# Kernel tuning notes

Measured on AMD Instinct MI355X. Metric: run time of the kernel, lower is better.

Reference implementation:

```python
import jax, jax.numpy as jnp
import numpy as np

C = 1.0          # curvature
ALPHA = 0.2      # LeakyReLU negative slope
MIN_NORM = 1e-15
MASK_VAL = -9e15

def artanh(x):
    x = jnp.clip(x, -1 + 1e-7, 1 - 1e-7)
    return 0.5 * (jnp.log1p(x) - jnp.log1p(-x))

def logmap0(x, c):
    sqrt_c = jnp.sqrt(c)
    norm = jnp.maximum(jnp.linalg.norm(x, axis=-1, keepdims=True), MIN_NORM)
    return x / (sqrt_c * norm) * artanh(sqrt_c * norm)

def expmap0(u, c):
    sqrt_c = jnp.sqrt(c)
    norm = jnp.maximum(jnp.linalg.norm(u, axis=-1, keepdims=True), MIN_NORM)
    return jnp.tanh(sqrt_c * norm) * u / (sqrt_c * norm)

def proj(x, c):
    norm = jnp.maximum(jnp.linalg.norm(x, axis=-1, keepdims=True), MIN_NORM)
    maxnorm = (1.0 - 1e-5) / jnp.sqrt(c)
    return jnp.where(norm > maxnorm, x / norm * maxnorm, x)

def setup_inputs() -> dict:
    key = jax.random.key(0)
    k1, k2, k3, k4, k5 = jax.random.split(key, 5)
    N, D, CLS = 8192, 128, 16
    # points on the Poincare ball (small norm, then projected)
    x = proj(jax.random.normal(k1, (N, D), jnp.float32) * 0.01, C)
    # sparse-ish adjacency, avg degree ~32, with self loops
    adj = jax.random.uniform(k2, (N, N)) < (32.0 / N)
    adj = adj | jnp.eye(N, dtype=bool)
    W = jax.random.normal(k3, (D, CLS), jnp.float32) * (1.0 / np.sqrt(D))
    b = jnp.zeros((CLS,), jnp.float32)
    a_src = jax.random.normal(k4, (CLS,), jnp.float32) * 0.1
    a_dst = jax.random.normal(k5, (CLS,), jnp.float32) * 0.1
    return {"x": x, "adj": adj, "W": W, "b": b, "a_src": a_src, "a_dst": a_dst}

def reference(x, adj, W, b, a_src, a_dst):
    # hyperbolic -> tangent space at origin, then linear map to n_classes
    h = logmap0(x, C) @ W + b                              # [N, CLS]
    # GAT scores: e_ij = LeakyReLU(a_src.h_i + a_dst.h_j)
    e = jax.nn.leaky_relu((h @ a_src)[:, None] + (h @ a_dst)[None, :], ALPHA)  # [N, N]
    e = jnp.where(adj, e, MASK_VAL)
    att = jax.nn.softmax(e, axis=-1)                       # row softmax over neighbors
    out = jax.nn.elu(att @ h)                              # aggregate + activation
    # back onto the manifold
    return proj(expmap0(out, C), C)
```

## Files before the change

### kernel.cpp

```cpp
#include <hip/hip_runtime.h>
#include <math.h>

#define NN   8192
#define DD   128
#define CLS  16
#define ALPHA 0.2f
#define MAXD 1024

__global__ void adj_probe(const unsigned char* __restrict__ adj, int* flag)
{
    const int lane = threadIdx.x & 63;
    const int i = lane + 1;
    const int ok = ((i & 3) != 0) && (adj[(size_t)i * (NN + 1)] != 0);
    unsigned long long b = __ballot(ok);
    if (threadIdx.x == 0) *flag = (__popcll(b) > 24) ? 1 : 0;
}

__global__ __launch_bounds__(256) void hat_feat(
    const float* __restrict__ x, const float* __restrict__ W,
    const float* __restrict__ b, const float* __restrict__ a_src,
    const float* __restrict__ a_dst,
    float* __restrict__ h, float* __restrict__ s, float* __restrict__ dv)
{
    const int lane = threadIdx.x & 63;
    const int row  = (blockIdx.x << 2) + (threadIdx.x >> 6);

    const float* xr = x + (size_t)row * DD;
    float x0 = xr[lane];
    float x1 = xr[lane + 64];

    float nsq = x0 * x0 + x1 * x1;
    #pragma unroll
    for (int o = 32; o > 0; o >>= 1) nsq += __shfl_xor(nsq, o);

    float norm = fmaxf(sqrtf(nsq), 1e-15f);
    float t    = fminf(norm, 1.0f - 1e-7f);
    float art  = 0.5f * (log1pf(t) - log1pf(-t));
    float scl  = art / norm;
    x0 *= scl;
    x1 *= scl;

    float hc[CLS];
    #pragma unroll
    for (int c = 0; c < CLS; ++c)
        hc[c] = x0 * W[lane * CLS + c] + x1 * W[(lane + 64) * CLS + c];

    #pragma unroll
    for (int o = 32; o > 0; o >>= 1) {
        #pragma unroll
        for (int c = 0; c < CLS; ++c) hc[c] += __shfl_xor(hc[c], o);
    }

    float sv = 0.0f, dvv = 0.0f;
    #pragma unroll
    for (int c = 0; c < CLS; ++c) {
        hc[c] += b[c];
        sv  += hc[c] * a_src[c];
        dvv += hc[c] * a_dst[c];
    }

    if (lane == 0) {
        float* hr = h + (size_t)row * CLS;
        #pragma unroll
        for (int c = 0; c < CLS; ++c) hr[c] = hc[c];
        s[row]  = sv;
        dv[row] = dvv;
    }
}

__global__ __launch_bounds__(256) void hat_scan(
    const unsigned char* __restrict__ adj, const int* __restrict__ flag,
    int* __restrict__ nbr, int* __restrict__ cnt)
{
    const int lane = threadIdx.x & 63;
    const int row  = (blockIdx.x << 2) + (threadIdx.x >> 6);
    const bool bytemode = (*flag != 0);

    unsigned long long m0 = 0ull, m1 = 0ull;
    if (bytemode) {
        const uint4* arow = reinterpret_cast<const uint4*>(adj + (size_t)row * NN);
        #pragma unroll
        for (int it = 0; it < 8; ++it) {
            const uint4 a = arow[(it << 6) | lane];
            unsigned n0 = ((a.x & 0x01010101u) * 0x01020408u) >> 24;
            unsigned n1 = ((a.y & 0x01010101u) * 0x01020408u) >> 24;
            unsigned n2 = ((a.z & 0x01010101u) * 0x01020408u) >> 24;
            unsigned n3 = ((a.w & 0x01010101u) * 0x01020408u) >> 24;
            unsigned long long bits = (unsigned long long)(
                (n0 & 0xF) | ((n1 & 0xF) << 4) | ((n2 & 0xF) << 8) | ((n3 & 0xF) << 12));
            if (it < 4) m0 |= bits << (it << 4);
            else        m1 |= bits << ((it - 4) << 4);
        }
    } else {
        const uint4* arow = reinterpret_cast<const uint4*>(
            reinterpret_cast<const unsigned int*>(adj) + (size_t)row * NN);
        #pragma unroll
        for (int it = 0; it < 32; ++it) {
            const uint4 a = arow[(it << 6) | lane];
            unsigned long long bits =
                (unsigned long long)((a.x != 0u) | ((a.y != 0u) << 1) |
                                     ((a.z != 0u) << 2) | ((a.w != 0u) << 3));
            if (it < 16) m0 |= bits << (it << 2);
            else         m1 |= bits << ((it - 16) << 2);
        }
    }

    const int c = __popcll(m0) + __popcll(m1);
    int off = c;
    #pragma unroll
    for (int o = 1; o < 64; o <<= 1) {
        int v = __shfl_up(off, o);
        if (lane >= o) off += v;
    }
    const int total = __shfl(off, 63);
    off -= c;

    int* rbase = nbr + (size_t)row * MAXD;
    while (m0) {
        const int b = __builtin_ctzll(m0);
        m0 &= m0 - 1;
        const int j = bytemode ? (((b >> 4) << 10) | (lane << 4) | (b & 15))
                               : (((b >> 2) << 8)  | (lane << 2) | (b & 3));
        if (off < MAXD) rbase[off] = j;
        ++off;
    }
    while (m1) {
        const int b0 = __builtin_ctzll(m1);
        m1 &= m1 - 1;
        const int b = b0 + 64;
        const int j = bytemode ? (((b >> 4) << 10) | (lane << 4) | (b & 15))
                               : (((b >> 2) << 8)  | (lane << 2) | (b & 3));
        if (off < MAXD) rbase[off] = j;
        ++off;
    }
    if (lane == 0) cnt[row] = (total < MAXD) ? total : MAXD;
}

__global__ __launch_bounds__(256) void hat_agg(
    const float* __restrict__ h, const float* __restrict__ s,
    const float* __restrict__ dv, const int* __restrict__ nbr,
    const int* __restrict__ cnt, float* __restrict__ out)
{
    const int lane = threadIdx.x & 63;
    const int row  = (blockIdx.x << 2) + (threadIdx.x >> 6);
    const int cc   = lane & 15;
    const int g    = lane >> 4;

    const int n = cnt[row];
    const int* rbase = nbr + (size_t)row * MAXD;
    const float si = s[row];

    float mx = -3.0e38f;
    for (int i = lane; i < n; i += 64) {
        float e = si + dv[rbase[i]];
        e = (e > 0.0f) ? e : ALPHA * e;
        mx = fmaxf(mx, e);
    }
    #pragma unroll
    for (int o = 32; o > 0; o >>= 1) mx = fmaxf(mx, __shfl_xor(mx, o));

    float l = 0.0f, acc = 0.0f;
    #pragma unroll 2
    for (int base = 0; base < n; base += 4) {
        const int idx = base + g;
        if (idx < n) {
            const int j = rbase[idx];
            float e = si + dv[j];
            e = (e > 0.0f) ? e : ALPHA * e;
            const float w = __expf(e - mx);
            l += w;
            acc = fmaf(w, h[(size_t)j * CLS + cc], acc);
        }
    }
    l   += __shfl_xor(l, 16);   l   += __shfl_xor(l, 32);
    acc += __shfl_xor(acc, 16); acc += __shfl_xor(acc, 32);

    float* orow = out + (size_t)row * CLS;
    if (l > 0.0f) {
        float u = acc / l;
        u = (u > 0.0f) ? u : expm1f(u);
        float nsq = u * u;
        #pragma unroll
        for (int o = 8; o > 0; o >>= 1) nsq += __shfl_xor(nsq, o);
        float norm = fmaxf(sqrtf(nsq), 1e-15f);
        float th   = tanhf(norm);
        float sc2  = th / norm;
        const float maxnorm = 1.0f - 1e-5f;
        float sc3  = (th > maxnorm) ? (maxnorm / th) : 1.0f;
        if (lane < CLS) orow[lane] = u * sc2 * sc3;
    } else {
        if (lane < CLS) orow[lane] = 0.0f;
    }
}

extern "C" void kernel_launch(void* const* d_in, const int* in_sizes, int n_in,
                              void* d_out, int out_size, void* d_ws, size_t ws_size,
                              hipStream_t stream) {
    const float*         x     = (const float*)d_in[0];
    const unsigned char* adj   = (const unsigned char*)d_in[1];
    const float*         W     = (const float*)d_in[2];
    const float*         b     = (const float*)d_in[3];
    const float*         a_src = (const float*)d_in[4];
    const float*         a_dst = (const float*)d_in[5];
    float*               out   = (float*)d_out;

    float* h    = (float*)d_ws;
    float* s    = h + (size_t)NN * CLS;
    float* dv   = s + NN;
    int*   flag = (int*)(dv + NN);
    int*   cnt  = flag + 1;
    int*   nbr  = cnt + NN;

    adj_probe<<<1, 64, 0, stream>>>(adj, flag);
    hat_feat<<<NN / 4, 256, 0, stream>>>(x, W, b, a_src, a_dst, h, s, dv);
    hat_scan<<<NN / 4, 256, 0, stream>>>(adj, flag, nbr, cnt);
    hat_agg <<<NN / 4, 256, 0, stream>>>(h, s, dv, nbr, cnt, out);
}
```

Before: 72.20 us.

## Split adjacency row scan across four waves and fold probe into feature kernel

The adjacency scan now gives each row a full 256-thread block, with each wave handling a quarter of the row and writing to its own neighbor segment and count. This raises parallelism and memory-level concurrency for the scan, which reads the large adjacency matrix. The aggregation kernel walks the four segments in turn. The separate probe kernel is merged into the first block of the feature kernel to save one launch. Each segment holds at most 256 neighbors, so rows with a dense quarter would be truncated.

After: 69.17 us. 4.2% less time.

```diff
diff --git a/kernel.cpp b/kernel.cpp
--- a/kernel.cpp
+++ b/kernel.cpp
@@ -5,25 +5,24 @@
 #define DD   128
 #define CLS  16
 #define ALPHA 0.2f
-#define MAXD 1024
-
-__global__ void adj_probe(const unsigned char* __restrict__ adj, int* flag)
-{
-    const int lane = threadIdx.x & 63;
-    const int i = lane + 1;
-    const int ok = ((i & 3) != 0) && (adj[(size_t)i * (NN + 1)] != 0);
-    unsigned long long b = __ballot(ok);
-    if (threadIdx.x == 0) *flag = (__popcll(b) > 24) ? 1 : 0;
-}
+#define SEGCAP 256
 
 __global__ __launch_bounds__(256) void hat_feat(
     const float* __restrict__ x, const float* __restrict__ W,
     const float* __restrict__ b, const float* __restrict__ a_src,
-    const float* __restrict__ a_dst,
-    float* __restrict__ h, float* __restrict__ s, float* __restrict__ dv)
+    const float* __restrict__ a_dst, const unsigned char* __restrict__ adj,
+    float* __restrict__ h, float* __restrict__ s, float* __restrict__ dv,
+    int* __restrict__ flag)
 {
     const int lane = threadIdx.x & 63;
     const int row  = (blockIdx.x << 2) + (threadIdx.x >> 6);
+
+    if (blockIdx.x == 0 && threadIdx.x < 64) {
+        const int i = threadIdx.x + 1;
+        const int ok = ((i & 3) != 0) && (adj[(size_t)i * (NN + 1)] != 0);
+        unsigned long long bb = __ballot(ok);
+        if (threadIdx.x == 0) *flag = (__popcll(bb) > 24) ? 1 : 0;
+    }
 
     const float* xr = x + (size_t)row * DD;
     float x0 = xr[lane];
@@ -70,42 +69,41 @@
 
 __global__ __launch_bounds__(256) void hat_scan(
     const unsigned char* __restrict__ adj, const int* __restrict__ flag,
-    int* __restrict__ nbr, int* __restrict__ cnt)
+    int* __restrict__ nbr, int* __restrict__ cnt4)
 {
     const int lane = threadIdx.x & 63;
-    const int row  = (blockIdx.x << 2) + (threadIdx.x >> 6);
+    const int q    = threadIdx.x >> 6;
+    const int row  = blockIdx.x;
     const bool bytemode = (*flag != 0);
 
-    unsigned long long m0 = 0ull, m1 = 0ull;
+    unsigned mask = 0u;
     if (bytemode) {
-        const uint4* arow = reinterpret_cast<const uint4*>(adj + (size_t)row * NN);
-        #pragma unroll
-        for (int it = 0; it < 8; ++it) {
-            const uint4 a = arow[(it << 6) | lane];
+        const uint4* abase = reinterpret_cast<const uint4*>(
+            adj + (size_t)row * NN + q * 2048);
+        #pragma unroll
+        for (int it = 0; it < 2; ++it) {
+            const uint4 a = abase[(it << 6) | lane];
             unsigned n0 = ((a.x & 0x01010101u) * 0x01020408u) >> 24;
             unsigned n1 = ((a.y & 0x01010101u) * 0x01020408u) >> 24;
             unsigned n2 = ((a.z & 0x01010101u) * 0x01020408u) >> 24;
             unsigned n3 = ((a.w & 0x01010101u) * 0x01020408u) >> 24;
-            unsigned long long bits = (unsigned long long)(
-                (n0 & 0xF) | ((n1 & 0xF) << 4) | ((n2 & 0xF) << 8) | ((n3 & 0xF) << 12));
-            if (it < 4) m0 |= bits << (it << 4);
-            else        m1 |= bits << ((it - 4) << 4);
+            unsigned bits = (n0 & 0xF) | ((n1 & 0xF) << 4)
+                          | ((n2 & 0xF) << 8) | ((n3 & 0xF) << 12);
+            mask |= bits << (it << 4);
         }
     } else {
-        const uint4* arow = reinterpret_cast<const uint4*>(
-            reinterpret_cast<const unsigned int*>(adj) + (size_t)row * NN);
-        #pragma unroll
-        for (int it = 0; it < 32; ++it) {
-            const uint4 a = arow[(it << 6) | lane];
-            unsigned long long bits =
-                (unsigned long long)((a.x != 0u) | ((a.y != 0u) << 1) |
-                                     ((a.z != 0u) << 2) | ((a.w != 0u) << 3));
-            if (it < 16) m0 |= bits << (it << 2);
-            else         m1 |= bits << ((it - 16) << 2);
-        }
-    }
-
-    const int c = __popcll(m0) + __popcll(m1);
+        const uint4* abase = reinterpret_cast<const uint4*>(
+            reinterpret_cast<const unsigned int*>(adj) + (size_t)row * NN + q * 2048);
+        #pragma unroll
+        for (int it = 0; it < 8; ++it) {
+            const uint4 a = abase[(it << 6) | lane];
+            unsigned bits = (unsigned)(a.x != 0u)        | ((unsigned)(a.y != 0u) << 1)
+                          | ((unsigned)(a.z != 0u) << 2) | ((unsigned)(a.w != 0u) << 3);
+            mask |= bits << (it << 2);
+        }
+    }
+
+    const int c = __popc(mask);
     int off = c;
     #pragma unroll
     for (int o = 1; o < 64; o <<= 1) {
@@ -115,61 +113,62 @@
     const int total = __shfl(off, 63);
     off -= c;
 
-    int* rbase = nbr + (size_t)row * MAXD;
-    while (m0) {
-        const int b = __builtin_ctzll(m0);
-        m0 &= m0 - 1;
-        const int j = bytemode ? (((b >> 4) << 10) | (lane << 4) | (b & 15))
-                               : (((b >> 2) << 8)  | (lane << 2) | (b & 3));
-        if (off < MAXD) rbase[off] = j;
+    int* sb = nbr + ((size_t)row * 4 + q) * SEGCAP;
+    while (mask) {
+        const int b = __builtin_ctz(mask);
+        mask &= mask - 1;
+        const int j = bytemode
+            ? (q * 2048 + ((b >> 4) << 10) + (lane << 4) + (b & 15))
+            : (q * 2048 + ((b >> 2) << 8)  + (lane << 2) + (b & 3));
+        if (off < SEGCAP) sb[off] = j;
         ++off;
     }
-    while (m1) {
-        const int b0 = __builtin_ctzll(m1);
-        m1 &= m1 - 1;
-        const int b = b0 + 64;
-        const int j = bytemode ? (((b >> 4) << 10) | (lane << 4) | (b & 15))
-                               : (((b >> 2) << 8)  | (lane << 2) | (b & 3));
-        if (off < MAXD) rbase[off] = j;
-        ++off;
-    }
-    if (lane == 0) cnt[row] = (total < MAXD) ? total : MAXD;
+    if (lane == 0) cnt4[row * 4 + q] = (total < SEGCAP) ? total : SEGCAP;
 }
 
 __global__ __launch_bounds__(256) void hat_agg(
     const float* __restrict__ h, const float* __restrict__ s,
     const float* __restrict__ dv, const int* __restrict__ nbr,
-    const int* __restrict__ cnt, float* __restrict__ out)
+    const int* __restrict__ cnt4, float* __restrict__ out)
 {
     const int lane = threadIdx.x & 63;
     const int row  = (blockIdx.x << 2) + (threadIdx.x >> 6);
     const int cc   = lane & 15;
     const int g    = lane >> 4;
 
-    const int n = cnt[row];
-    const int* rbase = nbr + (size_t)row * MAXD;
     const float si = s[row];
+    const int4 nq = *reinterpret_cast<const int4*>(cnt4 + row * 4);
+    const int* rbase = nbr + (size_t)row * 4 * SEGCAP;
 
     float mx = -3.0e38f;
-    for (int i = lane; i < n; i += 64) {
-        float e = si + dv[rbase[i]];
-        e = (e > 0.0f) ? e : ALPHA * e;
-        mx = fmaxf(mx, e);
+    #pragma unroll
+    for (int q = 0; q < 4; ++q) {
+        const int n = (&nq.x)[q];
+        const int* sb = rbase + q * SEGCAP;
+        for (int i = lane; i < n; i += 64) {
+            float e = si + dv[sb[i]];
+            e = (e > 0.0f) ? e : ALPHA * e;
+            mx = fmaxf(mx, e);
+        }
     }
     #pragma unroll
     for (int o = 32; o > 0; o >>= 1) mx = fmaxf(mx, __shfl_xor(mx, o));
 
     float l = 0.0f, acc = 0.0f;
-    #pragma unroll 2
-    for (int base = 0; base < n; base += 4) {
-        const int idx = base + g;
-        if (idx < n) {
-            const int j = rbase[idx];
-            float e = si + dv[j];
-            e = (e > 0.0f) ? e : ALPHA * e;
-            const float w = __expf(e - mx);
-            l += w;
-            acc = fmaf(w, h[(size_t)j * CLS + cc], acc);
+    #pragma unroll
+    for (int q = 0; q < 4; ++q) {
+        const int n = (&nq.x)[q];
+        const int* sb = rbase + q * SEGCAP;
+        for (int base = 0; base < n; base += 4) {
+            const int idx = base + g;
+            if (idx < n) {
+                const int j = sb[idx];
+                float e = si + dv[j];
+                e = (e > 0.0f) ? e : ALPHA * e;
+                const float w = __expf(e - mx);
+                l += w;
+                acc = fmaf(w, h[(size_t)j * CLS + cc], acc);
+            }
         }
     }
     l   += __shfl_xor(l, 16);   l   += __shfl_xor(l, 32);
@@ -208,11 +207,10 @@
     float* s    = h + (size_t)NN * CLS;
     float* dv   = s + NN;
     int*   flag = (int*)(dv + NN);
-    int*   cnt  = flag + 1;
-    int*   nbr  = cnt + NN;
-
-    adj_probe<<<1, 64, 0, stream>>>(adj, flag);
-    hat_feat<<<NN / 4, 256, 0, stream>>>(x, W, b, a_src, a_dst, h, s, dv);
-    hat_scan<<<NN / 4, 256, 0, stream>>>(adj, flag, nbr, cnt);
-    hat_agg <<<NN / 4, 256, 0, stream>>>(h, s, dv, nbr, cnt, out);
-}
+    int*   cnt4 = flag + 1;
+    int*   nbr  = cnt4 + (size_t)NN * 4;
+
+    hat_feat<<<NN / 4, 256, 0, stream>>>(x, W, b, a_src, a_dst, adj, h, s, dv, flag);
+    hat_scan<<<NN,     256, 0, stream>>>(adj, flag, nbr, cnt4);
+    hat_agg <<<NN / 4, 256, 0, stream>>>(h, s, dv, nbr, cnt4, out);
+}
```
